# Kernel optimization log

Hardware: AMD Instinct MI355X
Metric: run time of the kernel (lower is better)

## Reference

```python
import jax, jax.numpy as jnp
import numpy as np

DIM = 256
NUM_HEADS = 4
HEAD_DIM = DIM // NUM_HEADS  # 64
SCALE = HEAD_DIM ** -0.5


def _dwconv(x, w, b):
    # x: [B,H,W,C], w: [3,3,1,C] depthwise, stride 2, padding 1
    c = x.shape[-1]
    y = jax.lax.conv_general_dilated(
        x, w, window_strides=(2, 2), padding=((1, 1), (1, 1)),
        dimension_numbers=('NHWC', 'HWIO', 'NHWC'), feature_group_count=c)
    return y + b


def setup_inputs() -> dict:
    key = jax.random.key(0)
    ks = jax.random.split(key, 12)
    s = 0.02
    return {
        'x': jax.random.normal(ks[0], (8, 64, 64, DIM), jnp.float32),
        'q_w': jax.random.normal(ks[1], (DIM, DIM), jnp.float32) * s,
        'q_b': jnp.zeros((DIM,), jnp.float32),
        'k_w': jax.random.normal(ks[2], (DIM, HEAD_DIM), jnp.float32) * s,
        'k_b': jnp.zeros((HEAD_DIM,), jnp.float32),
        'v_w': jax.random.normal(ks[3], (DIM, HEAD_DIM), jnp.float32) * s,
        'v_b': jnp.zeros((HEAD_DIM,), jnp.float32),
        'kconv_w': jax.random.normal(ks[4], (3, 3, 1, HEAD_DIM), jnp.float32) * s,
        'kconv_b': jnp.zeros((HEAD_DIM,), jnp.float32),
        'vconv_w': jax.random.normal(ks[5], (3, 3, 1, HEAD_DIM), jnp.float32) * s,
        'vconv_b': jnp.zeros((HEAD_DIM,), jnp.float32),
        'out_w': jax.random.normal(ks[6], (DIM, DIM), jnp.float32) * s,
        'out_b': jnp.zeros((DIM,), jnp.float32),
    }


def reference(x, q_w, q_b, k_w, k_b, v_w, v_b,
              kconv_w, kconv_b, vconv_w, vconv_b, out_w, out_b):
    B, H, W, _ = x.shape
    S = H * W
    q = x @ q_w + q_b                      # [B,H,W,DIM]
    k = x @ k_w + k_b                      # [B,H,W,HEAD_DIM]
    v = x @ v_w + v_b
    k = _dwconv(k, kconv_w, kconv_b)       # [B,H/2,W/2,HEAD_DIM]
    v = _dwconv(v, vconv_w, vconv_b)
    Kv = (H // 2) * (W // 2)
    q = q.reshape(B, S, NUM_HEADS, HEAD_DIM)
    k = k.reshape(B, Kv, HEAD_DIM)
    v = v.reshape(B, Kv, HEAD_DIM)
    # MQA: single shared K/V head
    attn = jnp.einsum('bqhd,bkd->bhqk', q, k) * SCALE
    attn = jax.nn.softmax(attn, axis=-1)
    out = jnp.einsum('bhqk,bkd->bqhd', attn, v)   # [B,S,nh,hd]
    out = out.reshape(B, S, DIM) @ out_w + out_b
    return out.reshape(B, H, W, DIM)
```

## Files before the change

### kernel.cpp

```cpp
#include <hip/hip_runtime.h>
#include <hip/hip_bf16.h>

typedef __bf16 v8bf __attribute__((ext_vector_type(8)));
typedef float f32x4 __attribute__((ext_vector_type(4)));
typedef float f32x16 __attribute__((ext_vector_type(16)));
typedef int v2i __attribute__((ext_vector_type(2)));
typedef int v4i __attribute__((ext_vector_type(4)));

#define MFMA16(a, b, c) __builtin_amdgcn_mfma_f32_16x16x32_bf16(a, b, c, 0, 0, 0)
#define MFMA32(a, b, c) __builtin_amdgcn_mfma_f32_32x32x16_bf16(a, b, c, 0, 0, 0)
#define GLOAD16(gp, lp)                                                        \
  __builtin_amdgcn_global_load_lds(                                            \
      (const __attribute__((address_space(1))) void*)(gp),                     \
      (__attribute__((address_space(3))) void*)(lp), 16, 0, 0)

#define QSCALE 0.18033688011112042f

__global__ __launch_bounds__(256) void k_cvt_w(const float* __restrict__ qw,
                                               const float* __restrict__ kw,
                                               const float* __restrict__ vw,
                                               const float* __restrict__ ow,
                                               __bf16* __restrict__ wfrag,
                                               __bf16* __restrict__ owfrag) {
  int t = blockIdx.x * 256 + threadIdx.x;
  if (t < 98304) {
    int e = t & 7, idx = t >> 3;
    int l = idx & 63; idx >>= 6;
    int n = idx & 3; idx >>= 2;
    int kk = idx & 7, nb = idx >> 3;
    int nn = nb * 64 + n * 16 + (l & 15);
    int k = kk * 32 + 8 * (l >> 4) + e;
    float v;
    if (nn < 256) v = qw[k * 256 + nn] * QSCALE;
    else if (nn < 320) v = kw[k * 64 + (nn - 256)];
    else v = vw[k * 64 + (nn - 320)];
    wfrag[t] = (__bf16)v;
  } else {
    int u = t - 98304;
    int e = u & 7, idx = u >> 3;
    int l = idx & 63; idx >>= 6;
    int n = idx & 3; idx >>= 2;
    int kk = idx & 7, nb = idx >> 3;
    int nn = nb * 64 + n * 16 + (l & 15);
    int k = kk * 32 + 8 * (l >> 4) + e;
    owfrag[u] = (__bf16)ow[k * 256 + nn];
  }
}

__global__ __launch_bounds__(256) void k_qkv(const float* __restrict__ x,
                                             const __bf16* __restrict__ wfrag,
                                             const float* __restrict__ qb,
                                             const float* __restrict__ kb,
                                             const float* __restrict__ vb,
                                             __bf16* __restrict__ qo,
                                             __bf16* __restrict__ klin,
                                             __bf16* __restrict__ vlin) {
  int bx = blockIdx.x;
  int mb = (bx & 7) * 128 + (bx >> 3);
  int wave = threadIdx.x >> 6, lane = threadIdx.x & 63;
  int rg = wave >> 1, nh = wave & 1;
  int g = lane >> 4, c = lane & 15;
  int r0 = mb * 32 + rg * 16;
  const v8bf* wf = (const v8bf*)wfrag;

  v8bf a[8];
#pragma unroll
  for (int kk = 0; kk < 8; ++kk) {
    const float* ap = x + (size_t)(r0 + c) * 256 + kk * 32 + 8 * g;
    float4 f0 = *(const float4*)ap;
    float4 f1 = *(const float4*)(ap + 4);
    v8bf t;
    t[0] = (__bf16)f0.x; t[1] = (__bf16)f0.y; t[2] = (__bf16)f0.z; t[3] = (__bf16)f0.w;
    t[4] = (__bf16)f1.x; t[5] = (__bf16)f1.y; t[6] = (__bf16)f1.z; t[7] = (__bf16)f1.w;
    a[kk] = t;
  }
#pragma unroll
  for (int ni = 0; ni < 3; ++ni) {
    int nb = nh * 3 + ni;
    int n0 = nb * 64;
    f32x4 acc[4];
#pragma unroll
    for (int n = 0; n < 4; ++n) acc[n] = f32x4{0.f, 0.f, 0.f, 0.f};
#pragma unroll
    for (int kk = 0; kk < 8; ++kk) {
      v8bf bf[4];
#pragma unroll
      for (int n = 0; n < 4; ++n)
        bf[n] = wf[(((nb * 8 + kk) * 4 + n) << 6) | lane];
#pragma unroll
      for (int n = 0; n < 4; ++n) acc[n] = MFMA16(a[kk], bf[n], acc[n]);
    }
#pragma unroll
    for (int n = 0; n < 4; ++n) {
      int col = n0 + n * 16 + c;
      float bias;
      if (col < 256) bias = qb[col] * QSCALE;
      else if (col < 320) bias = kb[col - 256];
      else bias = vb[col - 320];
#pragma unroll
      for (int j = 0; j < 4; ++j) {
        int row = r0 + 4 * g + j;
        float v = acc[n][j] + bias;
        if (col < 256) qo[(size_t)row * 256 + col] = (__bf16)v;
        else if (col < 320) klin[(size_t)row * 64 + (col - 256)] = (__bf16)v;
        else vlin[(size_t)row * 64 + (col - 320)] = (__bf16)v;
      }
    }
  }
}

__global__ __launch_bounds__(256) void k_conv(const __bf16* __restrict__ klin,
                                              const __bf16* __restrict__ vlin,
                                              const float* __restrict__ kw,
                                              const float* __restrict__ kbias,
                                              const float* __restrict__ vw,
                                              const float* __restrict__ vbias,
                                              __bf16* __restrict__ kcS,
                                              __bf16* __restrict__ vcS) {
  int bx = blockIdx.x;
  int phase = bx >> 8;
  int b = (bx >> 5) & 7, tile = bx & 31;
  int u = threadIdx.x;

  if (phase == 0) {
    const __bf16* kin = klin + (size_t)b * 262144;
    int kj = u >> 5, kr = (u & 31) ^ kj;
    float acc[8];
#pragma unroll
    for (int e = 0; e < 8; ++e) acc[e] = kbias[kj * 8 + e];
#pragma unroll
    for (int dy = 0; dy < 3; ++dy) {
      int iy = 2 * tile - 1 + dy;
      if (iy < 0 || iy > 63) continue;
#pragma unroll
      for (int dx = 0; dx < 3; ++dx) {
        int ix = 2 * kr - 1 + dx;
        if (ix < 0 || ix > 63) continue;
        v8bf kv8 = *(const v8bf*)(kin + ((size_t)iy * 64 + ix) * 64 + kj * 8);
        const float* wp = kw + (dy * 3 + dx) * 64 + kj * 8;
#pragma unroll
        for (int e = 0; e < 8; ++e) acc[e] += (float)kv8[e] * wp[e];
      }
    }
    __bf16 o[8];
#pragma unroll
    for (int e = 0; e < 8; ++e) o[e] = (__bf16)acc[e];
    *(v4i*)(kcS + ((size_t)b * 32 + tile) * 2048 + u * 8) = *(v4i*)o;
  } else {
    const __bf16* vin = vlin + (size_t)b * 262144;
    int dt = u >> 7, ks = (u >> 6) & 1, vh = (u >> 5) & 1;
    int cc = (u & 31) ^ (ks * 2 + vh);
    int ch = dt * 32 + cc;
    float vwv[9];
#pragma unroll
    for (int i = 0; i < 9; ++i) vwv[i] = vw[i * 64 + ch];
    float vb0 = vbias[ch];
    __bf16 o[8];
#pragma unroll
    for (int e = 0; e < 8; ++e) {
      int ox = ks * 16 + vh * 8 + e;
      float av = vb0;
#pragma unroll
      for (int dy = 0; dy < 3; ++dy) {
        int iy = 2 * tile - 1 + dy;
        if (iy < 0 || iy > 63) continue;
#pragma unroll
        for (int dx = 0; dx < 3; ++dx) {
          int ix = 2 * ox - 1 + dx;
          if (ix < 0 || ix > 63) continue;
          av += (float)vin[((size_t)iy * 64 + ix) * 64 + ch] * vwv[dy * 3 + dx];
        }
      }
      o[e] = (__bf16)av;
    }
    *(v4i*)(vcS + ((size_t)b * 32 + tile) * 2048 + u * 8) = *(v4i*)o;
  }
}

__global__ __launch_bounds__(512, 4) void k_attn(const __bf16* __restrict__ q,
                                                 const __bf16* __restrict__ kcS,
                                                 const __bf16* __restrict__ vcS,
                                                 const __bf16* __restrict__ owfrag,
                                                 const float* __restrict__ ob,
                                                 float* __restrict__ out) {
  __shared__ __bf16 SMEM[16896];
  int bx = blockIdx.x;
  int L = (bx & 7) * 64 + (bx >> 3);
  int b = L >> 6, qt = L & 63;
  int tid = threadIdx.x;
  int wave = tid >> 6, lane = tid & 63;
  int h = wave & 3, rg = wave >> 2;
  int c = lane & 31, hi = lane >> 5;
  size_t rowBase = (size_t)b * 4096 + qt * 64;

  const __bf16* gsrc = (tid < 256)
                           ? kcS + (size_t)b * 65536 + tid * 8
                           : vcS + (size_t)b * 65536 + (tid - 256) * 8;
  __bf16* ldst = (tid < 256) ? &SMEM[tid * 8] : &SMEM[2048 + (tid - 256) * 8];

  int Koff[4], Voff[2][2];
#pragma unroll
  for (int kk = 0; kk < 4; ++kk) {
    int j = kk * 2 + hi;
    Koff[kk] = (j * 32 + (c ^ j)) * 8;
  }
#pragma unroll
  for (int ks = 0; ks < 2; ++ks)
#pragma unroll
    for (int dt = 0; dt < 2; ++dt) {
      int j = ks * 2 + hi;
      Voff[ks][dt] = (256 + dt * 128 + ks * 64 + hi * 32 + (c ^ j)) * 8;
    }

  const __bf16* qbase = q + (rowBase + rg * 32 + c) * 256 + h * 64 + hi * 8;
  v8bf Qf[4];
#pragma unroll
  for (int kk = 0; kk < 4; ++kk) Qf[kk] = *(const v8bf*)(qbase + kk * 16);

  f32x16 O0 = {}, O1 = {};
  const f32x16 Z16 = {};
  float ls0 = 0.f, ls1 = 0.f, ls2 = 0.f, ls3 = 0.f;

  GLOAD16(gsrc, ldst);
  GLOAD16(gsrc + 2048, ldst + 4096);

  int cur = 0;
  int nxt2 = 2;
  for (int it = 0; it < 32; ++it) {
    if (it < 31) {
      asm volatile("s_waitcnt vmcnt(1)" ::: "memory");
    } else {
      asm volatile("s_waitcnt vmcnt(0)" ::: "memory");
    }
    __builtin_amdgcn_sched_barrier(0);
    __builtin_amdgcn_s_barrier();
    __builtin_amdgcn_sched_barrier(0);
    if (it < 30) {
      GLOAD16(gsrc + (it + 2) * 2048, ldst + nxt2 * 4096);
    }

    const __bf16* base = &SMEM[cur * 4096];
    v8bf Kf[4], Vf[2][2];
#pragma unroll
    for (int kk = 0; kk < 4; ++kk) Kf[kk] = *(const v8bf*)(base + Koff[kk]);
#pragma unroll
    for (int ks = 0; ks < 2; ++ks)
#pragma unroll
      for (int dt = 0; dt < 2; ++dt)
        Vf[ks][dt] = *(const v8bf*)(base + Voff[ks][dt]);

    f32x16 S = MFMA32(Kf[0], Qf[0], Z16);
    S = MFMA32(Kf[1], Qf[1], S);
    S = MFMA32(Kf[2], Qf[2], S);
    S = MFMA32(Kf[3], Qf[3], S);

#pragma unroll
    for (int r = 0; r < 16; ++r) S[r] = __builtin_amdgcn_exp2f(S[r]);
    ls0 += (S[0] + S[1]) + (S[2] + S[3]);
    ls1 += (S[4] + S[5]) + (S[6] + S[7]);
    ls2 += (S[8] + S[9]) + (S[10] + S[11]);
    ls3 += (S[12] + S[13]) + (S[14] + S[15]);

    int w[8];
#pragma unroll
    for (int q2 = 0; q2 < 8; ++q2) {
      int r;
      asm("v_cvt_pk_bf16_f32 %0, %1, %2"
          : "=v"(r) : "v"(S[2 * q2]), "v"(S[2 * q2 + 1]));
      w[q2] = r;
    }
    v2i s1 = __builtin_amdgcn_permlane32_swap(w[2], w[0], false, false);
    v2i s2 = __builtin_amdgcn_permlane32_swap(w[3], w[1], false, false);
    v2i s3 = __builtin_amdgcn_permlane32_swap(w[6], w[4], false, false);
    v2i s4 = __builtin_amdgcn_permlane32_swap(w[7], w[5], false, false);
    v4i pa0i, pa1i;
    pa0i[0] = s1[1]; pa0i[1] = s2[1]; pa0i[2] = s1[0]; pa0i[3] = s2[0];
    pa1i[0] = s3[1]; pa1i[1] = s4[1]; pa1i[2] = s3[0]; pa1i[3] = s4[0];
    v8bf pa0 = *(v8bf*)&pa0i, pa1 = *(v8bf*)&pa1i;

    O0 = MFMA32(pa0, Vf[0][0], O0);
    O1 = MFMA32(pa0, Vf[0][1], O1);
    O0 = MFMA32(pa1, Vf[1][0], O0);
    O1 = MFMA32(pa1, Vf[1][1], O1);

    cur = (cur == 2) ? 0 : cur + 1;
    nxt2 = (nxt2 == 2) ? 0 : nxt2 + 1;
  }

  float lsum = (ls0 + ls1) + (ls2 + ls3);
  float tot = lsum + __shfl_xor(lsum, 32);
  float linv = 1.0f / tot;

  __syncthreads();

  __bf16(*Ot)[264] = (__bf16(*)[264])SMEM;
#pragma unroll
  for (int r = 0; r < 16; ++r) {
    int qr = (r & 3) + 8 * (r >> 2) + 4 * hi;
    float li = __shfl(linv, qr);
    Ot[rg * 32 + qr][h * 64 + c] = (__bf16)(O0[r] * li);
    Ot[rg * 32 + qr][h * 64 + 32 + c] = (__bf16)(O1[r] * li);
  }
  __syncthreads();

  int g = lane >> 4, c16 = lane & 15;
  const v8bf* wf = (const v8bf*)owfrag;
  f32x4 acc[2][4];
#pragma unroll
  for (int m = 0; m < 2; ++m)
#pragma unroll
    for (int n = 0; n < 4; ++n) acc[m][n] = f32x4{0.f, 0.f, 0.f, 0.f};
#pragma unroll
  for (int kk = 0; kk < 8; ++kk) {
    v8bf a0 = *(const v8bf*)&Ot[rg * 32 + c16][kk * 32 + 8 * g];
    v8bf a1 = *(const v8bf*)&Ot[rg * 32 + 16 + c16][kk * 32 + 8 * g];
    v8bf bf[4];
#pragma unroll
    for (int n = 0; n < 4; ++n)
      bf[n] = wf[(((h * 8 + kk) * 4 + n) << 6) | lane];
#pragma unroll
    for (int n = 0; n < 4; ++n) {
      acc[0][n] = MFMA16(a0, bf[n], acc[0][n]);
      acc[1][n] = MFMA16(a1, bf[n], acc[1][n]);
    }
  }
#pragma unroll
  for (int n = 0; n < 4; ++n) {
    int col = h * 64 + n * 16 + c16;
    float bias = ob[col];
#pragma unroll
    for (int m = 0; m < 2; ++m)
#pragma unroll
      for (int j = 0; j < 4; ++j) {
        int row = rg * 32 + m * 16 + 4 * g + j;
        out[(rowBase + row) * 256 + col] = acc[m][n][j] + bias;
      }
  }
}

extern "C" void kernel_launch(void* const* d_in, const int* in_sizes, int n_in,
                              void* d_out, int out_size, void* d_ws, size_t ws_size,
                              hipStream_t stream) {
  const float* x   = (const float*)d_in[0];
  const float* qw  = (const float*)d_in[1];
  const float* qb  = (const float*)d_in[2];
  const float* kw  = (const float*)d_in[3];
  const float* kb  = (const float*)d_in[4];
  const float* vw  = (const float*)d_in[5];
  const float* vb  = (const float*)d_in[6];
  const float* kcw = (const float*)d_in[7];
  const float* kcb = (const float*)d_in[8];
  const float* vcw = (const float*)d_in[9];
  const float* vcb = (const float*)d_in[10];
  const float* ow  = (const float*)d_in[11];
  const float* ob  = (const float*)d_in[12];
  float* out = (float*)d_out;
  char* ws = (char*)d_ws;

  __bf16* kcS    = (__bf16*)(ws + 0);
  __bf16* vcS    = (__bf16*)(ws + 1048576);
  __bf16* qbuf   = (__bf16*)(ws + 16777216);
  __bf16* klin   = (__bf16*)(ws + 33554432);
  __bf16* vlin   = (__bf16*)(ws + 37748736);
  __bf16* wfrag  = (__bf16*)(ws + 44040192);
  __bf16* owfrag = (__bf16*)(ws + 44236800);

  k_cvt_w<<<640, 256, 0, stream>>>(qw, kw, vw, ow, wfrag, owfrag);
  k_qkv<<<1024, 256, 0, stream>>>(x, wfrag, qb, kb, vb, qbuf, klin, vlin);
  k_conv<<<512, 256, 0, stream>>>(klin, vlin, kcw, kcb, vcw, vcb, kcS, vcS);
  k_attn<<<512, 512, 0, stream>>>(qbuf, kcS, vcS, owfrag, ob, out);
}
```

Before: 86.32 us.

## Split QKV and conv kernels into finer blocks for more parallelism

```diff
diff --git a/kernel.cpp b/kernel.cpp
--- a/kernel.cpp
+++ b/kernel.cpp
@@ -56,11 +56,10 @@
                                              __bf16* __restrict__ klin,
                                              __bf16* __restrict__ vlin) {
   int bx = blockIdx.x;
-  int mb = (bx & 7) * 128 + (bx >> 3);
+  int mb = (bx & 7) * 256 + (bx >> 3);
   int wave = threadIdx.x >> 6, lane = threadIdx.x & 63;
-  int rg = wave >> 1, nh = wave & 1;
   int g = lane >> 4, c = lane & 15;
-  int r0 = mb * 32 + rg * 16;
+  int r0 = mb * 16;
   const v8bf* wf = (const v8bf*)wfrag;
 
   v8bf a[8];
@@ -74,37 +73,34 @@
     t[4] = (__bf16)f1.x; t[5] = (__bf16)f1.y; t[6] = (__bf16)f1.z; t[7] = (__bf16)f1.w;
     a[kk] = t;
   }
-#pragma unroll
-  for (int ni = 0; ni < 3; ++ni) {
-    int nb = nh * 3 + ni;
-    int n0 = nb * 64;
-    f32x4 acc[4];
-#pragma unroll
-    for (int n = 0; n < 4; ++n) acc[n] = f32x4{0.f, 0.f, 0.f, 0.f};
-#pragma unroll
-    for (int kk = 0; kk < 8; ++kk) {
-      v8bf bf[4];
-#pragma unroll
-      for (int n = 0; n < 4; ++n)
-        bf[n] = wf[(((nb * 8 + kk) * 4 + n) << 6) | lane];
-#pragma unroll
-      for (int n = 0; n < 4; ++n) acc[n] = MFMA16(a[kk], bf[n], acc[n]);
-    }
-#pragma unroll
-    for (int n = 0; n < 4; ++n) {
-      int col = n0 + n * 16 + c;
-      float bias;
-      if (col < 256) bias = qb[col] * QSCALE;
-      else if (col < 320) bias = kb[col - 256];
-      else bias = vb[col - 320];
-#pragma unroll
-      for (int j = 0; j < 4; ++j) {
-        int row = r0 + 4 * g + j;
-        float v = acc[n][j] + bias;
-        if (col < 256) qo[(size_t)row * 256 + col] = (__bf16)v;
-        else if (col < 320) klin[(size_t)row * 64 + (col - 256)] = (__bf16)v;
-        else vlin[(size_t)row * 64 + (col - 320)] = (__bf16)v;
-      }
+  f32x4 acc[6];
+#pragma unroll
+  for (int i = 0; i < 6; ++i) acc[i] = f32x4{0.f, 0.f, 0.f, 0.f};
+#pragma unroll
+  for (int kk = 0; kk < 8; ++kk) {
+    v8bf bf[6];
+#pragma unroll
+    for (int i = 0; i < 6; ++i) {
+      int cf = wave * 6 + i;
+      bf[i] = wf[((((cf >> 2) * 8 + kk) * 4 + (cf & 3)) << 6) | lane];
+    }
+#pragma unroll
+    for (int i = 0; i < 6; ++i) acc[i] = MFMA16(a[kk], bf[i], acc[i]);
+  }
+#pragma unroll
+  for (int i = 0; i < 6; ++i) {
+    int col = (wave * 6 + i) * 16 + c;
+    float bias;
+    if (col < 256) bias = qb[col] * QSCALE;
+    else if (col < 320) bias = kb[col - 256];
+    else bias = vb[col - 320];
+#pragma unroll
+    for (int j = 0; j < 4; ++j) {
+      int row = r0 + 4 * g + j;
+      float v = acc[i][j] + bias;
+      if (col < 256) qo[(size_t)row * 256 + col] = (__bf16)v;
+      else if (col < 320) klin[(size_t)row * 64 + (col - 256)] = (__bf16)v;
+      else vlin[(size_t)row * 64 + (col - 320)] = (__bf16)v;
     }
   }
 }
@@ -118,16 +114,18 @@
                                               __bf16* __restrict__ kcS,
                                               __bf16* __restrict__ vcS) {
   int bx = blockIdx.x;
-  int phase = bx >> 8;
-  int b = (bx >> 5) & 7, tile = bx & 31;
+  int phase = bx >> 9;
+  int sub = bx & 511;
+  int half = sub >> 8;
+  int b = (sub >> 5) & 7, tile = sub & 31;
   int u = threadIdx.x;
 
   if (phase == 0) {
     const __bf16* kin = klin + (size_t)b * 262144;
     int kj = u >> 5, kr = (u & 31) ^ kj;
-    float acc[8];
-#pragma unroll
-    for (int e = 0; e < 8; ++e) acc[e] = kbias[kj * 8 + e];
+    float acc[4];
+#pragma unroll
+    for (int e = 0; e < 4; ++e) acc[e] = kbias[kj * 8 + half * 4 + e];
 #pragma unroll
     for (int dy = 0; dy < 3; ++dy) {
       int iy = 2 * tile - 1 + dy;
@@ -137,15 +135,15 @@
         int ix = 2 * kr - 1 + dx;
         if (ix < 0 || ix > 63) continue;
         v8bf kv8 = *(const v8bf*)(kin + ((size_t)iy * 64 + ix) * 64 + kj * 8);
-        const float* wp = kw + (dy * 3 + dx) * 64 + kj * 8;
-#pragma unroll
-        for (int e = 0; e < 8; ++e) acc[e] += (float)kv8[e] * wp[e];
+        const float* wp = kw + (dy * 3 + dx) * 64 + kj * 8 + half * 4;
+#pragma unroll
+        for (int e = 0; e < 4; ++e) acc[e] += (float)kv8[half * 4 + e] * wp[e];
       }
     }
-    __bf16 o[8];
-#pragma unroll
-    for (int e = 0; e < 8; ++e) o[e] = (__bf16)acc[e];
-    *(v4i*)(kcS + ((size_t)b * 32 + tile) * 2048 + u * 8) = *(v4i*)o;
+    __bf16 o[4];
+#pragma unroll
+    for (int e = 0; e < 4; ++e) o[e] = (__bf16)acc[e];
+    *(v2i*)(kcS + ((size_t)b * 32 + tile) * 2048 + u * 8 + half * 4) = *(v2i*)o;
   } else {
     const __bf16* vin = vlin + (size_t)b * 262144;
     int dt = u >> 7, ks = (u >> 6) & 1, vh = (u >> 5) & 1;
@@ -155,10 +153,10 @@
 #pragma unroll
     for (int i = 0; i < 9; ++i) vwv[i] = vw[i * 64 + ch];
     float vb0 = vbias[ch];
-    __bf16 o[8];
-#pragma unroll
-    for (int e = 0; e < 8; ++e) {
-      int ox = ks * 16 + vh * 8 + e;
+    __bf16 o[4];
+#pragma unroll
+    for (int e = 0; e < 4; ++e) {
+      int ox = ks * 16 + vh * 8 + half * 4 + e;
       float av = vb0;
 #pragma unroll
       for (int dy = 0; dy < 3; ++dy) {
@@ -173,7 +171,7 @@
       }
       o[e] = (__bf16)av;
     }
-    *(v4i*)(vcS + ((size_t)b * 32 + tile) * 2048 + u * 8) = *(v4i*)o;
+    *(v2i*)(vcS + ((size_t)b * 32 + tile) * 2048 + u * 8 + half * 4) = *(v2i*)o;
   }
 }
 
@@ -366,7 +364,7 @@
   __bf16* owfrag = (__bf16*)(ws + 44236800);
 
   k_cvt_w<<<640, 256, 0, stream>>>(qw, kw, vw, ow, wfrag, owfrag);
-  k_qkv<<<1024, 256, 0, stream>>>(x, wfrag, qb, kb, vb, qbuf, klin, vlin);
-  k_conv<<<512, 256, 0, stream>>>(klin, vlin, kcw, kcb, vcw, vcb, kcS, vcS);
+  k_qkv<<<2048, 256, 0, stream>>>(x, wfrag, qb, kb, vb, qbuf, klin, vlin);
+  k_conv<<<1024, 256, 0, stream>>>(klin, vlin, kcw, kcb, vcw, vcb, kcS, vcS);
   k_attn<<<512, 512, 0, stream>>>(qbuf, kcS, vcS, owfrag, ob, out);
 }
```

Measured after the change: 91.31 us. +5.8%, slower.
